# Kernel optimization log

Measured on AMD Instinct MI355X. Metric: run time of the kernel, lower is better.

Reference implementation:

```python
import jax, jax.numpy as jnp
import numpy as np

H = 8
SPLIT = 1
# deterministic stand-in for random.shuffle(range(8)) in the original
_PERM = np.random.RandomState(0).permutation(H)
SERIES_IDX = jnp.asarray(_PERM[SPLIT:])  # 7 heads
CROSS_IDX = jnp.asarray(_PERM[:SPLIT])   # 1 head


def setup_inputs() -> dict:
    key = jax.random.key(0)
    ks = jax.random.split(key, 5)
    B, L, E = 8, 1024, 64
    shp = (B, L, H, E)
    return {
        "queries": jax.random.normal(ks[0], shp, dtype=jnp.float32),
        "keys": jax.random.normal(ks[1], shp, dtype=jnp.float32),
        "keysT": jax.random.normal(ks[2], shp, dtype=jnp.float32),
        "values": jax.random.normal(ks[3], shp, dtype=jnp.float32),
        "valuesT": jax.random.normal(ks[4], shp, dtype=jnp.float32),
    }


def reference(queries, keys, keysT, values, valuesT):
    B, L, _, E = queries.shape
    scale = 1.0 / jnp.sqrt(jnp.asarray(E, dtype=queries.dtype))
    neg_inf = jnp.asarray(-jnp.inf, dtype=queries.dtype)

    # head split (gather along head dim)
    sq = queries[:, :, SERIES_IDX]   # [B,L,7,E]
    sk = keys[:, :, SERIES_IDX]      # [B,S,7,E]
    sv = values[:, :, SERIES_IDX]    # [B,S,7,D]
    cq = queries[:, :, CROSS_IDX]    # [B,L,1,E]
    ckT = keysT[:, :, CROSS_IDX]     # [B,C,1,E]
    cvT = valuesT[:, :, CROSS_IDX]   # [B,C,1,D]

    # causal mask: True above the diagonal -> disallowed
    causal = jnp.triu(jnp.ones((L, L), dtype=bool), k=1)  # [L,L]

    # series branch
    scores = jnp.einsum('blne,bsne->bnls', sq, sk)  # [B,7,L,S]
    scores = jnp.where(causal[None, None], neg_inf, scores * scale)
    series = jax.nn.softmax(scores, axis=-1)
    V = jnp.einsum('bhls,bshd->blhd', series, sv)   # [B,L,7,D]

    # cross branch
    cscores = jnp.einsum('blme,bcme->bmlc', cq, ckT)  # [B,1,L,C]
    cscores = jnp.where(causal[None, None], neg_inf, cscores * scale)
    crosses = jax.nn.softmax(cscores, axis=-1)
    V_cross = jnp.einsum('bhlc,bchd->blhd', crosses, cvT)  # [B,L,1,D]

    return jnp.concatenate([V, V_cross], axis=2)  # [B,L,8,D]
```

## Files before the change

### kernel.cpp

```cpp
#include <hip/hip_runtime.h>
#include <math.h>

#define Lq 1024
#define Hq 8
#define Eq 64
#define LDW 72
#define KV_SH (64 * LDW)
#define BUF_SH (2 * KV_SH)

#define SRC_HEAD_PACKED 0x64503712u

#define KW_ELEMS (8u * 8u * 1024u * 64u)
#define WS_NEEDED ((size_t)2 * KW_ELEMS * sizeof(unsigned short))

typedef __bf16 bf16_t;
typedef __bf16 bf16x8 __attribute__((ext_vector_type(8)));
typedef __bf16 bf16x4 __attribute__((ext_vector_type(4)));
typedef short short4v __attribute__((ext_vector_type(4)));
typedef float floatx4 __attribute__((ext_vector_type(4)));

__device__ __forceinline__ bf16x8 cvt8(const float4 a, const float4 b) {
    bf16x8 r;
    r[0] = (bf16_t)a.x; r[1] = (bf16_t)a.y; r[2] = (bf16_t)a.z; r[3] = (bf16_t)a.w;
    r[4] = (bf16_t)b.x; r[5] = (bf16_t)b.y; r[6] = (bf16_t)b.z; r[7] = (bf16_t)b.w;
    return r;
}

__device__ __forceinline__ void block_sync_lds() {
    asm volatile("s_waitcnt lgkmcnt(0)" ::: "memory");
    __builtin_amdgcn_s_barrier();
    __builtin_amdgcn_sched_barrier(0);
}

__global__ __launch_bounds__(256, 2)
void prep_kv(const float* __restrict__ Ks, const float* __restrict__ KTs,
             const float* __restrict__ Vs, const float* __restrict__ VTs,
             unsigned short* __restrict__ Kw, unsigned short* __restrict__ Vw) {
    const int slot = blockIdx.x, b = blockIdx.y, lt = blockIdx.z;
    const int h = (SRC_HEAD_PACKED >> (slot * 4)) & 0xF;
    const float* __restrict__ Kp = (slot == 7) ? KTs : Ks;
    const float* __restrict__ Vp = (slot == 7) ? VTs : Vs;
    const int tid = threadIdx.x;
    const int row = tid >> 2, c0 = (tid & 3) * 16;

    {
        const float* kb = Kp + (((size_t)b * Lq + lt * 64 + row) * Hq + h) * Eq + c0;
        float4 f0 = ((const float4*)kb)[0], f1 = ((const float4*)kb)[1];
        float4 f2 = ((const float4*)kb)[2], f3 = ((const float4*)kb)[3];
        unsigned short* kd = Kw + (((size_t)slot * 8 + b) * Lq + lt * 64 + row) * Eq + c0;
        *(bf16x8*)kd       = cvt8(f0, f1);
        *(bf16x8*)(kd + 8) = cvt8(f2, f3);
    }
    __shared__ float vt[64][68];
    {
        const float* vb = Vp + (((size_t)b * Lq + lt * 64 + row) * Hq + h) * Eq + c0;
        *(float4*)&vt[row][c0]      = ((const float4*)vb)[0];
        *(float4*)&vt[row][c0 + 4]  = ((const float4*)vb)[1];
        *(float4*)&vt[row][c0 + 8]  = ((const float4*)vb)[2];
        *(float4*)&vt[row][c0 + 12] = ((const float4*)vb)[3];
    }
    __syncthreads();
    {
        const int d = row, l0 = c0;
        float4 g0, g1, g2, g3;
        g0.x = vt[l0 +  0][d]; g0.y = vt[l0 +  1][d]; g0.z = vt[l0 +  2][d]; g0.w = vt[l0 +  3][d];
        g1.x = vt[l0 +  4][d]; g1.y = vt[l0 +  5][d]; g1.z = vt[l0 +  6][d]; g1.w = vt[l0 +  7][d];
        g2.x = vt[l0 +  8][d]; g2.y = vt[l0 +  9][d]; g2.z = vt[l0 + 10][d]; g2.w = vt[l0 + 11][d];
        g3.x = vt[l0 + 12][d]; g3.y = vt[l0 + 13][d]; g3.z = vt[l0 + 14][d]; g3.w = vt[l0 + 15][d];
        unsigned short* vd = Vw + ((((size_t)slot * 8 + b) * 16 + lt) * 64 + d) * 64 + l0;
        *(bf16x8*)vd       = cvt8(g0, g1);
        *(bf16x8*)(vd + 8) = cvt8(g2, g3);
    }
}

__global__ __launch_bounds__(512, 4)
void attn_ws(const float* __restrict__ Q, const unsigned short* __restrict__ Kw,
             const unsigned short* __restrict__ Vw, float* __restrict__ out) {
    const int slot = blockIdx.x;
    const int b    = blockIdx.y;
    const int p    = blockIdx.z;
    const int h    = (SRC_HEAD_PACKED >> (slot * 4)) & 0xF;
    const int pA = p, pB = 15 - p;

    const int tid  = threadIdx.x;
    const int wv   = tid >> 6;
    const int lane = tid & 63;
    const int ln16 = lane & 15;
    const int quad = lane >> 4;
    const int tb   = wv >> 2;
    const int kh   = (wv >> 1) & 1;
    const int wh   = wv & 1;
    const int pT   = tb ? pB : pA;

    __shared__ alignas(16) unsigned short smem[2 * BUF_SH];

    const float qs = 0.125f * 1.44269504f;
    bf16x8 qf[2][2];
    #pragma unroll
    for (int qi = 0; qi < 2; ++qi) {
        const int qg = wh * 2 + qi;
        const int r = pT * 64 + qg * 16 + ln16;
        const float* qa = Q + (((size_t)b * Lq + r) * Hq + h) * Eq + quad * 8;
        #pragma unroll
        for (int ec = 0; ec < 2; ++ec) {
            float4 f0 = ((const float4*)(qa + ec * 32))[0];
            float4 f1 = ((const float4*)(qa + ec * 32))[1];
            f0.x*=qs; f0.y*=qs; f0.z*=qs; f0.w*=qs;
            f1.x*=qs; f1.y*=qs; f1.z*=qs; f1.w*=qs;
            qf[qi][ec] = cvt8(f0, f1);
        }
    }

    floatx4 O[2][4];
    #pragma unroll
    for (int qi = 0; qi < 2; ++qi)
        #pragma unroll
        for (int dc = 0; dc < 4; ++dc) O[qi][dc] = (floatx4){0, 0, 0, 0};
    float psl[2] = {0.f, 0.f};

    const unsigned short* kwb = Kw + ((size_t)slot * 8 + b) * Lq * Eq;
    const unsigned short* vwb = Vw + ((size_t)slot * 8 + b) * 16 * 4096;
    const int srow = tid >> 3, sc8 = (tid & 7) * 8;

    float4 kreg, vreg;
    auto load_tile = [&](int kt) {
        kreg = *(const float4*)(kwb + (size_t)kt * 4096 + tid * 8);
        vreg = *(const float4*)(vwb + (size_t)kt * 4096 + tid * 8);
    };
    auto stage = [&](int bsel) {
        unsigned short* dst = smem + bsel * BUF_SH;
        *(float4*)&dst[srow * LDW + sc8]         = kreg;
        *(float4*)&dst[KV_SH + srow * LDW + sc8] = vreg;
    };

    load_tile(0);
    stage(0);
    load_tile(1);
    block_sync_lds();

    for (int kt = 0; kt <= pB; ++kt) {
        const unsigned short* base = smem + (kt & 1) * BUF_SH;
        const bool act = (kt <= pT);

        bf16x8 kf[2][2];
        if (act) {
            #pragma unroll
            for (int c = 0; c < 2; ++c) {
                kf[c][0] = *(const bf16x8*)&base[((kh * 2 + c) * 16 + ln16) * LDW + quad * 8];
                kf[c][1] = *(const bf16x8*)&base[((kh * 2 + c) * 16 + ln16) * LDW + 32 + quad * 8];
            }
        }
        if (kt < pB) stage((kt + 1) & 1);
        if (kt + 1 < pB) load_tile(kt + 2);

        if (act) {
            bf16x4 va[4][2];
            #pragma unroll
            for (int dc = 0; dc < 4; ++dc)
                #pragma unroll
                for (int nc = 0; nc < 2; ++nc)
                    va[dc][nc] = *(const bf16x4*)&base[KV_SH + (dc * 16 + ln16) * LDW + kh * 32 + nc * 16 + quad * 4];

            const bool diag = (kt == pT);
            #pragma unroll
            for (int qi = 0; qi < 2; ++qi) {
                const int qg = wh * 2 + qi;
                if (diag && kh && wh == 0) continue;

                floatx4 s[2];
                #pragma unroll
                for (int nc = 0; nc < 2; ++nc) {
                    floatx4 acc = (floatx4){0, 0, 0, 0};
                    acc = __builtin_amdgcn_mfma_f32_16x16x32_bf16(kf[nc][0], qf[qi][0], acc, 0, 0, 0);
                    acc = __builtin_amdgcn_mfma_f32_16x16x32_bf16(kf[nc][1], qf[qi][1], acc, 0, 0, 0);
                    s[nc] = acc;
                }
                if (diag) {
                    const int rin = qg * 16 + ln16;
                    #pragma unroll
                    for (int nc = 0; nc < 2; ++nc)
                        #pragma unroll
                        for (int r = 0; r < 4; ++r)
                            if (kh * 32 + nc * 16 + quad * 4 + r > rin) s[nc][r] = -INFINITY;
                }
                float pv[2][4];
                float ps = 0.f;
                #pragma unroll
                for (int nc = 0; nc < 2; ++nc)
                    #pragma unroll
                    for (int r = 0; r < 4; ++r) {
                        pv[nc][r] = __builtin_amdgcn_exp2f(s[nc][r]);
                        ps += pv[nc][r];
                    }
                psl[qi] += ps;

                short4v pb[2];
                #pragma unroll
                for (int nc = 0; nc < 2; ++nc) {
                    bf16x4 t;
                    t[0] = (bf16_t)pv[nc][0]; t[1] = (bf16_t)pv[nc][1];
                    t[2] = (bf16_t)pv[nc][2]; t[3] = (bf16_t)pv[nc][3];
                    pb[nc] = __builtin_bit_cast(short4v, t);
                }
                #pragma unroll
                for (int dc = 0; dc < 4; ++dc)
                    #pragma unroll
                    for (int nc = 0; nc < 2; ++nc)
                        O[qi][dc] = __builtin_amdgcn_mfma_f32_16x16x16bf16_1k(
                            __builtin_bit_cast(short4v, va[dc][nc]), pb[nc], O[qi][dc], 0, 0, 0);
            }
        }
        block_sync_lds();
    }

    float lsum[2];
    #pragma unroll
    for (int qi = 0; qi < 2; ++qi) {
        float l = psl[qi];
        l += __shfl_xor(l, 16, 64);
        l += __shfl_xor(l, 32, 64);
        lsum[qi] = l;
    }
    float* mb = (float*)smem;
    if (kh) {
        #pragma unroll
        for (int qi = 0; qi < 2; ++qi) {
            const int qg = wh * 2 + qi;
            float* dst = mb + ((tb * 4 + qg) * 64 + lane) * 18;
            #pragma unroll
            for (int dc = 0; dc < 4; ++dc) {
                *(float2*)(dst + dc * 4)     = make_float2(O[qi][dc][0], O[qi][dc][1]);
                *(float2*)(dst + dc * 4 + 2) = make_float2(O[qi][dc][2], O[qi][dc][3]);
            }
            dst[16] = lsum[qi];
        }
    }
    __syncthreads();
    if (!kh) {
        #pragma unroll
        for (int qi = 0; qi < 2; ++qi) {
            const int qg = wh * 2 + qi;
            const float* src = mb + ((tb * 4 + qg) * 64 + lane) * 18;
            const float inv = 1.0f / (lsum[qi] + src[16]);
            const int row = pT * 64 + qg * 16 + ln16;
            float* op = out + (((size_t)b * Lq + row) * Hq + slot) * Eq + quad * 4;
            #pragma unroll
            for (int dc = 0; dc < 4; ++dc) {
                float4 o;
                o.x = (O[qi][dc][0] + src[dc * 4 + 0]) * inv;
                o.y = (O[qi][dc][1] + src[dc * 4 + 1]) * inv;
                o.z = (O[qi][dc][2] + src[dc * 4 + 2]) * inv;
                o.w = (O[qi][dc][3] + src[dc * 4 + 3]) * inv;
                *(float4*)(op + dc * 16) = o;
            }
        }
    }
}

__global__ __launch_bounds__(512, 4)
void attn_mfma(const float* __restrict__ Q, const float* __restrict__ Ks,
               const float* __restrict__ KTs, const float* __restrict__ Vs,
               const float* __restrict__ VTs, float* __restrict__ out) {
    const int slot = blockIdx.x;
    const int b    = blockIdx.y;
    const int p    = blockIdx.z;
    const int h    = (SRC_HEAD_PACKED >> (slot * 4)) & 0xF;
    const float* __restrict__ Kp = (slot == 7) ? KTs : Ks;
    const float* __restrict__ Vp = (slot == 7) ? VTs : Vs;
    const int pA = p, pB = 15 - p;

    const int tid  = threadIdx.x;
    const int wv   = tid >> 6;
    const int lane = tid & 63;
    const int ln16 = lane & 15;
    const int quad = lane >> 4;
    const int tb   = wv >> 2;
    const int kh   = (wv >> 1) & 1;
    const int wh   = wv & 1;
    const int pT   = tb ? pB : pA;

    __shared__ alignas(16) unsigned short smem[2 * BUF_SH];

    const float qs = 0.125f * 1.44269504f;
    bf16x8 qf[2][2];
    #pragma unroll
    for (int qi = 0; qi < 2; ++qi) {
        const int qg = wh * 2 + qi;
        const int r = pT * 64 + qg * 16 + ln16;
        const float* qa = Q + (((size_t)b * Lq + r) * Hq + h) * Eq + quad * 8;
        #pragma unroll
        for (int ec = 0; ec < 2; ++ec) {
            float4 f0 = ((const float4*)(qa + ec * 32))[0];
            float4 f1 = ((const float4*)(qa + ec * 32))[1];
            f0.x*=qs; f0.y*=qs; f0.z*=qs; f0.w*=qs;
            f1.x*=qs; f1.y*=qs; f1.z*=qs; f1.w*=qs;
            qf[qi][ec] = cvt8(f0, f1);
        }
    }

    floatx4 O[2][4];
    #pragma unroll
    for (int qi = 0; qi < 2; ++qi)
        #pragma unroll
        for (int dc = 0; dc < 4; ++dc) O[qi][dc] = (floatx4){0, 0, 0, 0};
    float psl[2] = {0.f, 0.f};

    float4 kq[2];
    float  vq[8];
    const int kj = tid >> 3, kc = (tid & 7) * 8;
    const int vd = tid & 63, vk = (tid >> 6) * 8;

    auto load_tile = [&](int kt) {
        const float* kb = Kp + (((size_t)b * Lq + kt * 64 + kj) * Hq + h) * Eq + kc;
        kq[0] = ((const float4*)kb)[0]; kq[1] = ((const float4*)kb)[1];
        const float* vb = Vp + (((size_t)b * Lq + kt * 64 + vk) * Hq + h) * Eq + vd;
        #pragma unroll
        for (int i = 0; i < 8; ++i) vq[i] = vb[(size_t)i * (Hq * Eq)];
    };
    auto stage = [&](int bsel) {
        unsigned short* dst = smem + bsel * BUF_SH;
        *(bf16x8*)&dst[kj * LDW + kc] = cvt8(kq[0], kq[1]);
        const float4* vq4 = (const float4*)vq;
        *(bf16x8*)&dst[KV_SH + vd * LDW + vk] = cvt8(vq4[0], vq4[1]);
    };

    load_tile(0);
    stage(0);
    load_tile(1);
    block_sync_lds();

    for (int kt = 0; kt <= pB; ++kt) {
        const unsigned short* base = smem + (kt & 1) * BUF_SH;
        const bool act = (kt <= pT);

        bf16x8 kf[2][2];
        if (act) {
            #pragma unroll
            for (int c = 0; c < 2; ++c) {
                kf[c][0] = *(const bf16x8*)&base[((kh * 2 + c) * 16 + ln16) * LDW + quad * 8];
                kf[c][1] = *(const bf16x8*)&base[((kh * 2 + c) * 16 + ln16) * LDW + 32 + quad * 8];
            }
        }
        if (kt < pB) stage((kt + 1) & 1);
        if (kt + 1 < pB) load_tile(kt + 2);

        if (act) {
            bf16x4 va[4][2];
            #pragma unroll
            for (int dc = 0; dc < 4; ++dc)
                #pragma unroll
                for (int nc = 0; nc < 2; ++nc)
                    va[dc][nc] = *(const bf16x4*)&base[KV_SH + (dc * 16 + ln16) * LDW + kh * 32 + nc * 16 + quad * 4];

            const bool diag = (kt == pT);
            #pragma unroll
            for (int qi = 0; qi < 2; ++qi) {
                const int qg = wh * 2 + qi;
                if (diag && kh && wh == 0) continue;
                floatx4 s[2];
                #pragma unroll
                for (int nc = 0; nc < 2; ++nc) {
                    floatx4 acc = (floatx4){0, 0, 0, 0};
                    acc = __builtin_amdgcn_mfma_f32_16x16x32_bf16(kf[nc][0], qf[qi][0], acc, 0, 0, 0);
                    acc = __builtin_amdgcn_mfma_f32_16x16x32_bf16(kf[nc][1], qf[qi][1], acc, 0, 0, 0);
                    s[nc] = acc;
                }
                if (diag) {
                    const int rin = qg * 16 + ln16;
                    #pragma unroll
                    for (int nc = 0; nc < 2; ++nc)
                        #pragma unroll
                        for (int r = 0; r < 4; ++r)
                            if (kh * 32 + nc * 16 + quad * 4 + r > rin) s[nc][r] = -INFINITY;
                }
                float pv[2][4];
                float ps = 0.f;
                #pragma unroll
                for (int nc = 0; nc < 2; ++nc)
                    #pragma unroll
                    for (int r = 0; r < 4; ++r) {
                        pv[nc][r] = __builtin_amdgcn_exp2f(s[nc][r]);
                        ps += pv[nc][r];
                    }
                psl[qi] += ps;
                short4v pb[2];
                #pragma unroll
                for (int nc = 0; nc < 2; ++nc) {
                    bf16x4 t;
                    t[0] = (bf16_t)pv[nc][0]; t[1] = (bf16_t)pv[nc][1];
                    t[2] = (bf16_t)pv[nc][2]; t[3] = (bf16_t)pv[nc][3];
                    pb[nc] = __builtin_bit_cast(short4v, t);
                }
                #pragma unroll
                for (int dc = 0; dc < 4; ++dc)
                    #pragma unroll
                    for (int nc = 0; nc < 2; ++nc)
                        O[qi][dc] = __builtin_amdgcn_mfma_f32_16x16x16bf16_1k(
                            __builtin_bit_cast(short4v, va[dc][nc]), pb[nc], O[qi][dc], 0, 0, 0);
            }
        }
        block_sync_lds();
    }

    float lsum[2];
    #pragma unroll
    for (int qi = 0; qi < 2; ++qi) {
        float l = psl[qi];
        l += __shfl_xor(l, 16, 64);
        l += __shfl_xor(l, 32, 64);
        lsum[qi] = l;
    }
    float* mbf = (float*)smem;
    if (kh) {
        #pragma unroll
        for (int qi = 0; qi < 2; ++qi) {
            const int qg = wh * 2 + qi;
            float* dst = mbf + ((tb * 4 + qg) * 64 + lane) * 18;
            #pragma unroll
            for (int dc = 0; dc < 4; ++dc) {
                *(float2*)(dst + dc * 4)     = make_float2(O[qi][dc][0], O[qi][dc][1]);
                *(float2*)(dst + dc * 4 + 2) = make_float2(O[qi][dc][2], O[qi][dc][3]);
            }
            dst[16] = lsum[qi];
        }
    }
    __syncthreads();
    if (!kh) {
        #pragma unroll
        for (int qi = 0; qi < 2; ++qi) {
            const int qg = wh * 2 + qi;
            const float* src = mbf + ((tb * 4 + qg) * 64 + lane) * 18;
            const float inv = 1.0f / (lsum[qi] + src[16]);
            const int row = pT * 64 + qg * 16 + ln16;
            float* op = out + (((size_t)b * Lq + row) * Hq + slot) * Eq + quad * 4;
            #pragma unroll
            for (int dc = 0; dc < 4; ++dc) {
                float4 o;
                o.x = (O[qi][dc][0] + src[dc * 4 + 0]) * inv;
                o.y = (O[qi][dc][1] + src[dc * 4 + 1]) * inv;
                o.z = (O[qi][dc][2] + src[dc * 4 + 2]) * inv;
                o.w = (O[qi][dc][3] + src[dc * 4 + 3]) * inv;
                *(float4*)(op + dc * 16) = o;
            }
        }
    }
}

extern "C" void kernel_launch(void* const* d_in, const int* in_sizes, int n_in,
                              void* d_out, int out_size, void* d_ws, size_t ws_size,
                              hipStream_t stream) {
    const float* queries = (const float*)d_in[0];
    const float* keys    = (const float*)d_in[1];
    const float* keysT   = (const float*)d_in[2];
    const float* values  = (const float*)d_in[3];
    const float* valuesT = (const float*)d_in[4];
    float* out = (float*)d_out;

    if (d_ws != nullptr && ws_size >= WS_NEEDED) {
        unsigned short* Kw = (unsigned short*)d_ws;
        unsigned short* Vw = Kw + KW_ELEMS;
        dim3 pgrid(Hq, 8, 16);
        dim3 pblock(256);
        prep_kv<<<pgrid, pblock, 0, stream>>>(keys, keysT, values, valuesT, Kw, Vw);
        dim3 agrid(Hq, 8, 8);
        dim3 ablock(512);
        attn_ws<<<agrid, ablock, 0, stream>>>(queries, Kw, Vw, out);
    } else {
        dim3 grid(Hq, 8, 8);
        dim3 block(512);
        attn_mfma<<<grid, block, 0, stream>>>(queries, keys, keysT, values, valuesT, out);
    }
}
```

Baseline: 128.2 us.

## Split attention block's query half across grid, halving block size

```diff
diff --git a/kernel.cpp b/kernel.cpp
--- a/kernel.cpp
+++ b/kernel.cpp
@@ -73,12 +73,13 @@
     }
 }
 
-__global__ __launch_bounds__(512, 4)
+__global__ __launch_bounds__(256, 4)
 void attn_ws(const float* __restrict__ Q, const unsigned short* __restrict__ Kw,
              const unsigned short* __restrict__ Vw, float* __restrict__ out) {
     const int slot = blockIdx.x;
     const int b    = blockIdx.y;
-    const int p    = blockIdx.z;
+    const int p    = blockIdx.z & 7;
+    const int qh   = blockIdx.z >> 3;
     const int h    = (SRC_HEAD_PACKED >> (slot * 4)) & 0xF;
     const int pA = p, pB = 15 - p;
 
@@ -87,9 +88,8 @@
     const int lane = tid & 63;
     const int ln16 = lane & 15;
     const int quad = lane >> 4;
-    const int tb   = wv >> 2;
-    const int kh   = (wv >> 1) & 1;
-    const int wh   = wv & 1;
+    const int tb   = wv >> 1;
+    const int kh   = wv & 1;
     const int pT   = tb ? pB : pA;
 
     __shared__ alignas(16) unsigned short smem[2 * BUF_SH];
@@ -98,7 +98,7 @@
     bf16x8 qf[2][2];
     #pragma unroll
     for (int qi = 0; qi < 2; ++qi) {
-        const int qg = wh * 2 + qi;
+        const int qg = qh * 2 + qi;
         const int r = pT * 64 + qg * 16 + ln16;
         const float* qa = Q + (((size_t)b * Lq + r) * Hq + h) * Eq + quad * 8;
         #pragma unroll
@@ -120,17 +120,21 @@
 
     const unsigned short* kwb = Kw + ((size_t)slot * 8 + b) * Lq * Eq;
     const unsigned short* vwb = Vw + ((size_t)slot * 8 + b) * 16 * 4096;
-    const int srow = tid >> 3, sc8 = (tid & 7) * 8;
-
-    float4 kreg, vreg;
+    const int srow = tid >> 2, sc16 = (tid & 3) * 16;
+
+    float4 kreg[2], vreg[2];
     auto load_tile = [&](int kt) {
-        kreg = *(const float4*)(kwb + (size_t)kt * 4096 + tid * 8);
-        vreg = *(const float4*)(vwb + (size_t)kt * 4096 + tid * 8);
+        const unsigned short* ks = kwb + (size_t)kt * 4096 + tid * 16;
+        kreg[0] = ((const float4*)ks)[0]; kreg[1] = ((const float4*)ks)[1];
+        const unsigned short* vs = vwb + (size_t)kt * 4096 + tid * 16;
+        vreg[0] = ((const float4*)vs)[0]; vreg[1] = ((const float4*)vs)[1];
     };
     auto stage = [&](int bsel) {
         unsigned short* dst = smem + bsel * BUF_SH;
-        *(float4*)&dst[srow * LDW + sc8]         = kreg;
-        *(float4*)&dst[KV_SH + srow * LDW + sc8] = vreg;
+        *(float4*)&dst[srow * LDW + sc16]             = kreg[0];
+        *(float4*)&dst[srow * LDW + sc16 + 8]         = kreg[1];
+        *(float4*)&dst[KV_SH + srow * LDW + sc16]     = vreg[0];
+        *(float4*)&dst[KV_SH + srow * LDW + sc16 + 8] = vreg[1];
     };
 
     load_tile(0);
@@ -164,8 +168,8 @@
             const bool diag = (kt == pT);
             #pragma unroll
             for (int qi = 0; qi < 2; ++qi) {
-                const int qg = wh * 2 + qi;
-                if (diag && kh && wh == 0) continue;
+                const int qg = qh * 2 + qi;
+                if (diag && kh && qh == 0) continue;
 
                 floatx4 s[2];
                 #pragma unroll
@@ -225,8 +229,7 @@
     if (kh) {
         #pragma unroll
         for (int qi = 0; qi < 2; ++qi) {
-            const int qg = wh * 2 + qi;
-            float* dst = mb + ((tb * 4 + qg) * 64 + lane) * 18;
+            float* dst = mb + ((tb * 2 + qi) * 64 + lane) * 18;
             #pragma unroll
             for (int dc = 0; dc < 4; ++dc) {
                 *(float2*)(dst + dc * 4)     = make_float2(O[qi][dc][0], O[qi][dc][1]);
@@ -239,8 +242,8 @@
     if (!kh) {
         #pragma unroll
         for (int qi = 0; qi < 2; ++qi) {
-            const int qg = wh * 2 + qi;
-            const float* src = mb + ((tb * 4 + qg) * 64 + lane) * 18;
+            const int qg = qh * 2 + qi;
+            const float* src = mb + ((tb * 2 + qi) * 64 + lane) * 18;
             const float inv = 1.0f / (lsum[qi] + src[16]);
             const int row = pT * 64 + qg * 16 + ln16;
             float* op = out + (((size_t)b * Lq + row) * Hq + slot) * Eq + quad * 4;
@@ -462,8 +465,8 @@
         dim3 pgrid(Hq, 8, 16);
         dim3 pblock(256);
         prep_kv<<<pgrid, pblock, 0, stream>>>(keys, keysT, values, valuesT, Kw, Vw);
-        dim3 agrid(Hq, 8, 8);
-        dim3 ablock(512);
+        dim3 agrid(Hq, 8, 16);
+        dim3 ablock(256);
         attn_ws<<<agrid, ablock, 0, stream>>>(queries, Kw, Vw, out);
     } else {
         dim3 grid(Hq, 8, 8);
```

Measured after the change: 176.7 us. +37.9%, slower.
